# Kernel tuning notes

Measured on AMD Instinct MI355X. Metric: run time of the kernel, lower is better.

## Reference

```python
import jax, jax.numpy as jnp
import numpy as np


def setup_inputs() -> dict:
    key = jax.random.key(0)
    k1, k2, k3 = jax.random.split(key, 3)
    B, IN, H, OUT = 2048, 4096, 4096, 1024
    x = jax.random.normal(k1, (B, IN), dtype=jnp.float32)
    fc1_weight = jax.random.randint(k2, (H, IN), 0, 2).astype(jnp.int32)
    fc2_weight = jax.random.randint(k3, (OUT, H), 0, 2).astype(jnp.int32)
    return {"x": x, "fc1_weight": fc1_weight, "fc2_weight": fc2_weight, "threshold": 2048}


def _binary_popcount_matmul(a, w):
    # a: (B, K) in {0,1}, w: (N, K) in {0,1}
    # matches = sum_k 1 - (a XOR w) = a@w.T + (1-a)@(1-w).T  (identical math,
    # avoids materializing the (B, N, K) XNOR tensor the naive code builds)
    return jnp.einsum('bk,nk->bn', a, w) + jnp.einsum('bk,nk->bn', 1 - a, 1 - w)


def reference(x, fc1_weight, fc2_weight, threshold):
    xb = (x.reshape(x.shape[0], -1) >= 0).astype(jnp.int32)   # binarize input
    pc1 = _binary_popcount_matmul(xb, fc1_weight)              # (B, H) popcounts
    act1 = (pc1 >= threshold).astype(jnp.int32)                # threshold activation
    pc2 = _binary_popcount_matmul(act1, fc2_weight)            # (B, OUT) popcounts
    return pc2
```

## Files before the change

kernel.cpp:

```cpp
#include <hip/hip_runtime.h>
#include <stdint.h>

typedef int v4i  __attribute__((ext_vector_type(4)));
typedef int v16i __attribute__((ext_vector_type(16)));

__device__ __forceinline__ void gload_lds16(const void* g, void* l) {
    __builtin_amdgcn_global_load_lds(
        (const __attribute__((address_space(1))) void*)g,
        (__attribute__((address_space(3))) void*)l, 16, 0, 0);
}

template<typename T, bool ISFLOAT>
__global__ __launch_bounds__(512)
void pack_frag(const T* __restrict__ in, int8_t* __restrict__ F, int K) {
    __shared__ int8_t lbuf[32 * 1040];
    const int t  = threadIdx.x;
    const int db = blockIdx.y;
    const int c0 = blockIdx.x << 10;

    #pragma unroll
    for (int p = 0; p < 16; ++p) {
        int idx = p * 512 + t;
        int row = idx >> 8, c4 = idx & 255;
        uint32_t b;
        if constexpr (ISFLOAT) {
            const float4 v = *(const float4*)(in + (size_t)(db * 32 + row) * K + c0 + c4 * 4);
            b =  (v.x >= 0.0f ? 0x01u : 0xFFu)
              | ((v.y >= 0.0f ? 0x01u : 0xFFu) << 8)
              | ((v.z >= 0.0f ? 0x01u : 0xFFu) << 16)
              | ((v.w >= 0.0f ? 0x01u : 0xFFu) << 24);
        } else {
            const int4 v = *(const int4*)(in + (size_t)(db * 32 + row) * K + c0 + c4 * 4);
            b =  (v.x ? 0x01u : 0xFFu)
              | ((v.y ? 0x01u : 0xFFu) << 8)
              | ((v.z ? 0x01u : 0xFFu) << 16)
              | ((v.w ? 0x01u : 0xFFu) << 24);
        }
        *(uint32_t*)(lbuf + row * 1040 + c4 * 4) = b;
    }
    __syncthreads();

    const int s  = t >> 4;
    const int l0 = (t & 15) * 4;
    const int KC = K >> 5;
    int8_t* dst = F + ((size_t)db * KC + blockIdx.x * 32 + s) * 1024;
    #pragma unroll
    for (int li = 0; li < 4; ++li) {
        int l = l0 + li;
        uint4 v = *(const uint4*)(lbuf + (l & 31) * 1040 + s * 32 + (l >> 5) * 16);
        *(uint4*)(dst + l * 16) = v;
    }
}

__global__ __launch_bounds__(512, 1)
void bnn_l1_opt(const int8_t* __restrict__ Af,
                const int8_t* __restrict__ Bf,
                const int* __restrict__ thr_ptr,
                int8_t* __restrict__ actf)
{
    constexpr int KC  = 128;
    constexpr int NKT = 64;
    constexpr uint32_t BUFSZ = 24576;

    __shared__ int8_t lds[4 * 24576];

    const int tid  = threadIdx.x;
    const int lane = tid & 63;
    const int wv   = tid >> 6;
    const int wr   = wv >> 2, wc = wv & 3;

    const int g   = blockIdx.x;
    const int idx = g >> 3;
    const int bn  = (g & 7) * 2 + (idx >> 4);
    const int bm  = idx & 15;

    const int8_t* gsrc[3];
    uint32_t loff[3];
    #pragma unroll
    for (int c = 0; c < 3; ++c) {
        int s = c * 512 + tid;
        if (s < 512) {
            int R = s >> 7, kk = (s >> 6) & 1, ln = s & 63;
            gsrc[c] = Af + ((size_t)(bm * 4 + R) * KC + kk) * 1024 + ln * 16;
            loff[c] = (uint32_t)s * 16;
        } else {
            int s2 = s - 512;
            int Cb = s2 >> 7, kk = (s2 >> 6) & 1, ln = s2 & 63;
            gsrc[c] = Bf + ((size_t)(bn * 8 + Cb) * KC + kk) * 1024 + ln * 16;
            loff[c] = 8192u + (uint32_t)s2 * 16;
        }
    }

    auto issue3 = [&](uint32_t bufo) {
        gload_lds16(gsrc[0], lds + bufo + loff[0]); gsrc[0] += 2048;
        gload_lds16(gsrc[1], lds + bufo + loff[1]); gsrc[1] += 2048;
        gload_lds16(gsrc[2], lds + bufo + loff[2]); gsrc[2] += 2048;
    };

    v16i acc[2][2];
    #pragma unroll
    for (int i = 0; i < 2; ++i)
        #pragma unroll
        for (int j = 0; j < 2; ++j) acc[i][j] = {};

    issue3(0);
    issue3(BUFSZ);
    issue3(2 * BUFSZ);

#define KT_BODY(KT, P)                                                         \
    {                                                                          \
        const int kt_ = (KT);                                                  \
        if (kt_ < NKT - 2)       asm volatile("s_waitcnt vmcnt(6)" ::: "memory"); \
        else if (kt_ == NKT - 2) asm volatile("s_waitcnt vmcnt(3)" ::: "memory"); \
        else                     asm volatile("s_waitcnt vmcnt(0)" ::: "memory"); \
        __builtin_amdgcn_sched_barrier(0);                                     \
        __builtin_amdgcn_s_barrier();                                          \
        __builtin_amdgcn_sched_barrier(0);                                     \
        const int8_t* Ab = lds + (P) * 24576 + wr * 4096 + lane * 16;          \
        const int8_t* Bb = lds + (P) * 24576 + 8192 + wc * 4096 + lane * 16;   \
        v4i a00 = *(const v4i*)(Ab + 0);                                       \
        v4i a01 = *(const v4i*)(Ab + 1024);                                    \
        v4i a10 = *(const v4i*)(Ab + 2048);                                    \
        v4i a11 = *(const v4i*)(Ab + 3072);                                    \
        v4i b00 = *(const v4i*)(Bb + 0);                                       \
        v4i b01 = *(const v4i*)(Bb + 1024);                                    \
        v4i b10 = *(const v4i*)(Bb + 2048);                                    \
        v4i b11 = *(const v4i*)(Bb + 3072);                                    \
        if (kt_ + 3 < NKT) issue3(((P) + 3) % 4 * 24576u);                     \
        __builtin_amdgcn_sched_barrier(0);                                     \
        asm volatile("s_waitcnt lgkmcnt(0)" ::: "memory");                     \
        __builtin_amdgcn_sched_barrier(0);                                     \
        __builtin_amdgcn_s_setprio(1);                                         \
        acc[0][0] = __builtin_amdgcn_mfma_i32_32x32x32_i8(a00, b00, acc[0][0], 0, 0, 0); \
        acc[0][1] = __builtin_amdgcn_mfma_i32_32x32x32_i8(a00, b10, acc[0][1], 0, 0, 0); \
        acc[1][0] = __builtin_amdgcn_mfma_i32_32x32x32_i8(a10, b00, acc[1][0], 0, 0, 0); \
        acc[1][1] = __builtin_amdgcn_mfma_i32_32x32x32_i8(a10, b10, acc[1][1], 0, 0, 0); \
        acc[0][0] = __builtin_amdgcn_mfma_i32_32x32x32_i8(a01, b01, acc[0][0], 0, 0, 0); \
        acc[0][1] = __builtin_amdgcn_mfma_i32_32x32x32_i8(a01, b11, acc[0][1], 0, 0, 0); \
        acc[1][0] = __builtin_amdgcn_mfma_i32_32x32x32_i8(a11, b01, acc[1][0], 0, 0, 0); \
        acc[1][1] = __builtin_amdgcn_mfma_i32_32x32x32_i8(a11, b11, acc[1][1], 0, 0, 0); \
        __builtin_amdgcn_s_setprio(0);                                         \
        __builtin_amdgcn_sched_barrier(0);                                     \
    }

    #pragma unroll 1
    for (int kt0 = 0; kt0 < NKT; kt0 += 4) {
        KT_BODY(kt0 + 0, 0)
        KT_BODY(kt0 + 1, 1)
        KT_BODY(kt0 + 2, 2)
        KT_BODY(kt0 + 3, 3)
    }
#undef KT_BODY

    __syncthreads();
    const int thr = *thr_ptr;
    int8_t* bits = lds;
    #pragma unroll
    for (int i = 0; i < 2; ++i)
        #pragma unroll
        for (int j = 0; j < 2; ++j) {
            int dimb = wr * 64 + i * 32 + 4 * (lane >> 5);
            int gcl  = wc * 64 + j * 32 + (lane & 31);
            #pragma unroll
            for (int reg = 0; reg < 16; ++reg) {
                int dl = dimb + (reg & 3) + 8 * (reg >> 2);
                int match = (4096 + acc[i][j][reg]) >> 1;
                bits[dl * 272 + gcl] = (match >= thr) ? (int8_t)1 : (int8_t)-1;
            }
        }
    __syncthreads();
    const int s    = tid >> 4;
    const int dblk = s >> 3, kcl = s & 7;
    const int l0   = (tid & 15) * 4;
    int8_t* dst = actf + ((size_t)(bm * 4 + dblk) * KC + bn * 8 + kcl) * 1024;
    #pragma unroll
    for (int li = 0; li < 4; ++li) {
        int l = l0 + li;
        uint4 v = *(const uint4*)(bits + (dblk * 32 + (l & 31)) * 272
                                       + kcl * 32 + (l >> 5) * 16);
        *(uint4*)(dst + l * 16) = v;
    }
}

template<int WN>
__global__ __launch_bounds__(256, 1)
void bnn_mfma2(const int8_t* __restrict__ Af,
               const int8_t* __restrict__ Bf,
               int* __restrict__ out, int Nout)
{
    constexpr int KC     = 128;
    constexpr int NKT    = 64;
    constexpr int NBB    = 2 * WN;
    constexpr int ASLOTS = 512;
    constexpr int BSLOTS = 128 * NBB;
    constexpr int SLOTS  = ASLOTS + BSLOTS;
    constexpr int NLD    = SLOTS / 256;
    constexpr uint32_t BUFSZ = (uint32_t)SLOTS * 16;

    __shared__ int8_t lds[3][SLOTS * 16];

    const int tid  = threadIdx.x;
    const int lane = tid & 63;
    const int wv   = tid >> 6;
    const int wr   = wv >> 1, wc = wv & 1;

    const int g   = blockIdx.x;
    const int idx = g >> 3;
    const int bn  = (g & 7) * 2 + (idx >> 4);
    const int bm  = idx & 15;

    const int8_t* gsrc[NLD];
    uint32_t ldoff[NLD];
    #pragma unroll
    for (int i = 0; i < NLD; ++i) {
        int sbase = wv * 64 + 256 * i;
        ldoff[i] = (uint32_t)sbase * 16;
        const int8_t* base;
        if (sbase < ASLOTS) {
            int R = sbase >> 7, C = (sbase >> 6) & 1;
            base = Af + ((size_t)(bm * 4 + R) * KC + C) * 1024;
        } else {
            int s = sbase - ASLOTS;
            int R = s >> 7, C = (s >> 6) & 1;
            base = Bf + ((size_t)(bn * NBB + R) * KC + C) * 1024;
        }
        gsrc[i] = base + lane * 16;
    }

    auto stage = [&](int buf) {
        #pragma unroll
        for (int i = 0; i < NLD; ++i) {
            gload_lds16(gsrc[i], (int8_t*)lds + (uint32_t)buf * BUFSZ + ldoff[i]);
            gsrc[i] += 2048;
        }
    };

    v16i acc[2][WN];
    #pragma unroll
    for (int i = 0; i < 2; ++i)
        #pragma unroll
        for (int j = 0; j < WN; ++j) acc[i][j] = {};

    stage(0);
    stage(1);

    int cur = 0, nxt = 2;
    #pragma unroll 1
    for (int kt = 0; kt < NKT; ++kt) {
        if (kt < NKT - 1) asm volatile("s_waitcnt vmcnt(3)" ::: "memory");
        else              asm volatile("s_waitcnt vmcnt(0)" ::: "memory");
        __builtin_amdgcn_sched_barrier(0);
        __builtin_amdgcn_s_barrier();
        __builtin_amdgcn_sched_barrier(0);

        if (kt < NKT - 2) {
            stage(nxt);
            nxt = (nxt == 2) ? 0 : nxt + 1;
        }

        const int8_t* Al = lds[cur];
        const int8_t* Bl = lds[cur] + ASLOTS * 16;
        #pragma unroll
        for (int kc = 0; kc < 2; ++kc) {
            v4i af[2], bf[WN];
            #pragma unroll
            for (int i = 0; i < 2; ++i)
                af[i] = *(const v4i*)(Al + (((wr * 2 + i) * 2 + kc) * 64 + lane) * 16);
            #pragma unroll
            for (int j = 0; j < WN; ++j)
                bf[j] = *(const v4i*)(Bl + (((wc * WN + j) * 2 + kc) * 64 + lane) * 16);
            #pragma unroll
            for (int i = 0; i < 2; ++i)
                #pragma unroll
                for (int j = 0; j < WN; ++j)
                    acc[i][j] = __builtin_amdgcn_mfma_i32_32x32x32_i8(af[i], bf[j], acc[i][j], 0, 0, 0);
        }
        cur = (cur == 2) ? 0 : cur + 1;
    }

    #pragma unroll
    for (int i = 0; i < 2; ++i)
        #pragma unroll
        for (int j = 0; j < WN; ++j) {
            int gc = bn * (64 * WN) + wc * (32 * WN) + j * 32 + (lane & 31);
            #pragma unroll
            for (int reg = 0; reg < 16; ++reg) {
                int gr = bm * 128 + wr * 64 + i * 32
                       + (reg & 3) + 8 * (reg >> 2) + 4 * (lane >> 5);
                out[(size_t)gr * Nout + gc] = (4096 + acc[i][j][reg]) >> 1;
            }
        }
}

extern "C" void kernel_launch(void* const* d_in, const int* in_sizes, int n_in,
                              void* d_out, int out_size, void* d_ws, size_t ws_size,
                              hipStream_t stream) {
    const float* x   = (const float*)d_in[0];
    const int*   w1  = (const int*)d_in[1];
    const int*   w2  = (const int*)d_in[2];
    const int*   thr = (const int*)d_in[3];
    int* out = (int*)d_out;

    const int B = 2048, IN = 4096, H = 4096, OUT = 1024;
    uint8_t* ws = (uint8_t*)d_ws;

    int8_t* Af  = (int8_t*)(ws);
    int8_t* W1f = (int8_t*)(ws + ((size_t)8  << 20));
    int8_t* W2f = (int8_t*)(ws + ((size_t)24 << 20));
    int8_t* Act = (int8_t*)(ws + ((size_t)28 << 20));

    pack_frag<float, true ><<<dim3(IN / 1024, B   / 32), 512, 0, stream>>>(x,  Af,  IN);
    pack_frag<int,   false><<<dim3(IN / 1024, H   / 32), 512, 0, stream>>>(w1, W1f, IN);
    pack_frag<int,   false><<<dim3(H  / 1024, OUT / 32), 512, 0, stream>>>(w2, W2f, H);

    bnn_l1_opt<<<256, 512, 0, stream>>>(Af, W1f, thr, Act);
    bnn_mfma2<1><<<256, 256, 0, stream>>>(Act, W2f, out, OUT);
}
```

Before: 88.15 us.

## Retile layer-1 GEMM to 2-wave 128x128 blocks and halve pack_frag chunk

Layer-1 popcount GEMM moves from 512-thread blocks with 8 waves computing 256x128 tiles to 128-thread blocks with 2 waves, each wave computing 64x128 so that every A fragment is reused across 4 B fragments. The grid doubles to 512 blocks with 2 blocks per CU, and the LDS pipeline drops from 4 buffers to 3. The pack kernels now process 512-column chunks, launching twice as many smaller blocks with a simpler transpose. This trades fewer waves per CU and more accumulator registers for higher per-wave MFMA density and fewer barrier stalls, at some risk to latency hiding.

```diff
diff --git a/kernel.cpp b/kernel.cpp
--- a/kernel.cpp
+++ b/kernel.cpp
@@ -13,15 +13,15 @@
 template<typename T, bool ISFLOAT>
 __global__ __launch_bounds__(512)
 void pack_frag(const T* __restrict__ in, int8_t* __restrict__ F, int K) {
-    __shared__ int8_t lbuf[32 * 1040];
+    __shared__ int8_t lbuf[32 * 528];
     const int t  = threadIdx.x;
     const int db = blockIdx.y;
-    const int c0 = blockIdx.x << 10;
-
-    #pragma unroll
-    for (int p = 0; p < 16; ++p) {
+    const int c0 = blockIdx.x << 9;
+
+    #pragma unroll
+    for (int p = 0; p < 8; ++p) {
         int idx = p * 512 + t;
-        int row = idx >> 8, c4 = idx & 255;
+        int row = idx >> 7, c4 = idx & 127;
         uint32_t b;
         if constexpr (ISFLOAT) {
             const float4 v = *(const float4*)(in + (size_t)(db * 32 + row) * K + c0 + c4 * 4);
@@ -36,49 +36,46 @@
               | ((v.z ? 0x01u : 0xFFu) << 16)
               | ((v.w ? 0x01u : 0xFFu) << 24);
         }
-        *(uint32_t*)(lbuf + row * 1040 + c4 * 4) = b;
+        *(uint32_t*)(lbuf + row * 528 + c4 * 4) = b;
     }
     __syncthreads();
 
-    const int s  = t >> 4;
-    const int l0 = (t & 15) * 4;
+    const int s  = t >> 5;
+    const int l0 = t & 31;
     const int KC = K >> 5;
-    int8_t* dst = F + ((size_t)db * KC + blockIdx.x * 32 + s) * 1024;
-    #pragma unroll
-    for (int li = 0; li < 4; ++li) {
-        int l = l0 + li;
-        uint4 v = *(const uint4*)(lbuf + (l & 31) * 1040 + s * 32 + (l >> 5) * 16);
-        *(uint4*)(dst + l * 16) = v;
-    }
-}
-
-__global__ __launch_bounds__(512, 1)
-void bnn_l1_opt(const int8_t* __restrict__ Af,
-                const int8_t* __restrict__ Bf,
-                const int* __restrict__ thr_ptr,
-                int8_t* __restrict__ actf)
+    int8_t* dst = F + ((size_t)db * KC + (c0 >> 5) + s) * 1024;
+    uint4 v0 = *(const uint4*)(lbuf + l0 * 528 + s * 32);
+    uint4 v1 = *(const uint4*)(lbuf + l0 * 528 + s * 32 + 16);
+    *(uint4*)(dst + l0 * 16) = v0;
+    *(uint4*)(dst + (l0 + 32) * 16) = v1;
+}
+
+__global__ __launch_bounds__(128, 2)
+void bnn_l1_2w(const int8_t* __restrict__ Af,
+               const int8_t* __restrict__ Bf,
+               const int* __restrict__ thr_ptr,
+               int8_t* __restrict__ actf)
 {
     constexpr int KC  = 128;
     constexpr int NKT = 64;
-    constexpr uint32_t BUFSZ = 24576;
-
-    __shared__ int8_t lds[4 * 24576];
+    constexpr uint32_t BUFSZ = 16384;
+
+    __shared__ int8_t lds[3 * 16384];
 
     const int tid  = threadIdx.x;
     const int lane = tid & 63;
-    const int wv   = tid >> 6;
-    const int wr   = wv >> 2, wc = wv & 3;
+    const int wr   = tid >> 6;
 
     const int g   = blockIdx.x;
     const int idx = g >> 3;
-    const int bn  = (g & 7) * 2 + (idx >> 4);
+    const int bn  = (g & 7) * 4 + (idx >> 4);
     const int bm  = idx & 15;
 
-    const int8_t* gsrc[3];
-    uint32_t loff[3];
-    #pragma unroll
-    for (int c = 0; c < 3; ++c) {
-        int s = c * 512 + tid;
+    const int8_t* gsrc[8];
+    uint32_t loff[8];
+    #pragma unroll
+    for (int c = 0; c < 8; ++c) {
+        int s = c * 128 + tid;
         if (s < 512) {
             int R = s >> 7, kk = (s >> 6) & 1, ln = s & 63;
             gsrc[c] = Af + ((size_t)(bm * 4 + R) * KC + kk) * 1024 + ln * 16;
@@ -86,70 +83,77 @@
         } else {
             int s2 = s - 512;
             int Cb = s2 >> 7, kk = (s2 >> 6) & 1, ln = s2 & 63;
-            gsrc[c] = Bf + ((size_t)(bn * 8 + Cb) * KC + kk) * 1024 + ln * 16;
+            gsrc[c] = Bf + ((size_t)(bn * 4 + Cb) * KC + kk) * 1024 + ln * 16;
             loff[c] = 8192u + (uint32_t)s2 * 16;
         }
     }
-
-    auto issue3 = [&](uint32_t bufo) {
-        gload_lds16(gsrc[0], lds + bufo + loff[0]); gsrc[0] += 2048;
-        gload_lds16(gsrc[1], lds + bufo + loff[1]); gsrc[1] += 2048;
-        gload_lds16(gsrc[2], lds + bufo + loff[2]); gsrc[2] += 2048;
+    auto issue8 = [&](uint32_t bufo) {
+        #pragma unroll
+        for (int c = 0; c < 8; ++c) {
+            gload_lds16(gsrc[c], lds + bufo + loff[c]);
+            gsrc[c] += 2048;
+        }
     };
 
-    v16i acc[2][2];
+    v16i acc[2][4];
     #pragma unroll
     for (int i = 0; i < 2; ++i)
         #pragma unroll
-        for (int j = 0; j < 2; ++j) acc[i][j] = {};
-
-    issue3(0);
-    issue3(BUFSZ);
-    issue3(2 * BUFSZ);
+        for (int j = 0; j < 4; ++j) acc[i][j] = {};
+
+    issue8(0);
+    issue8(BUFSZ);
 
 #define KT_BODY(KT, P)                                                         \
     {                                                                          \
         const int kt_ = (KT);                                                  \
-        if (kt_ < NKT - 2)       asm volatile("s_waitcnt vmcnt(6)" ::: "memory"); \
-        else if (kt_ == NKT - 2) asm volatile("s_waitcnt vmcnt(3)" ::: "memory"); \
-        else                     asm volatile("s_waitcnt vmcnt(0)" ::: "memory"); \
+        if (kt_ < NKT - 1) asm volatile("s_waitcnt vmcnt(8)" ::: "memory");    \
+        else               asm volatile("s_waitcnt vmcnt(0)" ::: "memory");    \
         __builtin_amdgcn_sched_barrier(0);                                     \
         __builtin_amdgcn_s_barrier();                                          \
         __builtin_amdgcn_sched_barrier(0);                                     \
-        const int8_t* Ab = lds + (P) * 24576 + wr * 4096 + lane * 16;          \
-        const int8_t* Bb = lds + (P) * 24576 + 8192 + wc * 4096 + lane * 16;   \
+        const int8_t* Ab = lds + (P) * 16384 + wr * 4096 + lane * 16;          \
+        const int8_t* Bb = lds + (P) * 16384 + 8192 + lane * 16;               \
         v4i a00 = *(const v4i*)(Ab + 0);                                       \
         v4i a01 = *(const v4i*)(Ab + 1024);                                    \
         v4i a10 = *(const v4i*)(Ab + 2048);                                    \
         v4i a11 = *(const v4i*)(Ab + 3072);                                    \
-        v4i b00 = *(const v4i*)(Bb + 0);                                       \
-        v4i b01 = *(const v4i*)(Bb + 1024);                                    \
-        v4i b10 = *(const v4i*)(Bb + 2048);                                    \
-        v4i b11 = *(const v4i*)(Bb + 3072);                                    \
-        if (kt_ + 3 < NKT) issue3(((P) + 3) % 4 * 24576u);                     \
+        v4i b00 = *(const v4i*)(Bb + 0);    v4i b0k = *(const v4i*)(Bb + 1024);\
+        v4i b10 = *(const v4i*)(Bb + 2048); v4i b1k = *(const v4i*)(Bb + 3072);\
+        v4i b20 = *(const v4i*)(Bb + 4096); v4i b2k = *(const v4i*)(Bb + 5120);\
+        v4i b30 = *(const v4i*)(Bb + 6144); v4i b3k = *(const v4i*)(Bb + 7168);\
+        if (kt_ + 2 < NKT) issue8((uint32_t)(((P) + 2) % 3) * 16384u);         \
         __builtin_amdgcn_sched_barrier(0);                                     \
         asm volatile("s_waitcnt lgkmcnt(0)" ::: "memory");                     \
         __builtin_amdgcn_sched_barrier(0);                                     \
         __builtin_amdgcn_s_setprio(1);                                         \
         acc[0][0] = __builtin_amdgcn_mfma_i32_32x32x32_i8(a00, b00, acc[0][0], 0, 0, 0); \
         acc[0][1] = __builtin_amdgcn_mfma_i32_32x32x32_i8(a00, b10, acc[0][1], 0, 0, 0); \
+        acc[0][2] = __builtin_amdgcn_mfma_i32_32x32x32_i8(a00, b20, acc[0][2], 0, 0, 0); \
+        acc[0][3] = __builtin_amdgcn_mfma_i32_32x32x32_i8(a00, b30, acc[0][3], 0, 0, 0); \
         acc[1][0] = __builtin_amdgcn_mfma_i32_32x32x32_i8(a10, b00, acc[1][0], 0, 0, 0); \
         acc[1][1] = __builtin_amdgcn_mfma_i32_32x32x32_i8(a10, b10, acc[1][1], 0, 0, 0); \
-        acc[0][0] = __builtin_amdgcn_mfma_i32_32x32x32_i8(a01, b01, acc[0][0], 0, 0, 0); \
-        acc[0][1] = __builtin_amdgcn_mfma_i32_32x32x32_i8(a01, b11, acc[0][1], 0, 0, 0); \
-        acc[1][0] = __builtin_amdgcn_mfma_i32_32x32x32_i8(a11, b01, acc[1][0], 0, 0, 0); \
-        acc[1][1] = __builtin_amdgcn_mfma_i32_32x32x32_i8(a11, b11, acc[1][1], 0, 0, 0); \
+        acc[1][2] = __builtin_amdgcn_mfma_i32_32x32x32_i8(a10, b20, acc[1][2], 0, 0, 0); \
+        acc[1][3] = __builtin_amdgcn_mfma_i32_32x32x32_i8(a10, b30, acc[1][3], 0, 0, 0); \
+        acc[0][0] = __builtin_amdgcn_mfma_i32_32x32x32_i8(a01, b0k, acc[0][0], 0, 0, 0); \
+        acc[0][1] = __builtin_amdgcn_mfma_i32_32x32x32_i8(a01, b1k, acc[0][1], 0, 0, 0); \
+        acc[0][2] = __builtin_amdgcn_mfma_i32_32x32x32_i8(a01, b2k, acc[0][2], 0, 0, 0); \
+        acc[0][3] = __builtin_amdgcn_mfma_i32_32x32x32_i8(a01, b3k, acc[0][3], 0, 0, 0); \
+        acc[1][0] = __builtin_amdgcn_mfma_i32_32x32x32_i8(a11, b0k, acc[1][0], 0, 0, 0); \
+        acc[1][1] = __builtin_amdgcn_mfma_i32_32x32x32_i8(a11, b1k, acc[1][1], 0, 0, 0); \
+        acc[1][2] = __builtin_amdgcn_mfma_i32_32x32x32_i8(a11, b2k, acc[1][2], 0, 0, 0); \
+        acc[1][3] = __builtin_amdgcn_mfma_i32_32x32x32_i8(a11, b3k, acc[1][3], 0, 0, 0); \
         __builtin_amdgcn_s_setprio(0);                                         \
         __builtin_amdgcn_sched_barrier(0);                                     \
     }
 
     #pragma unroll 1
-    for (int kt0 = 0; kt0 < NKT; kt0 += 4) {
+    for (int kt0 = 0; kt0 < 63; kt0 += 3) {
         KT_BODY(kt0 + 0, 0)
         KT_BODY(kt0 + 1, 1)
         KT_BODY(kt0 + 2, 2)
-        KT_BODY(kt0 + 3, 3)
-    }
+    }
+    KT_BODY(63, 0)
 #undef KT_BODY
 
     __syncthreads();
@@ -158,25 +162,25 @@
     #pragma unroll
     for (int i = 0; i < 2; ++i)
         #pragma unroll
-        for (int j = 0; j < 2; ++j) {
+        for (int j = 0; j < 4; ++j) {
             int dimb = wr * 64 + i * 32 + 4 * (lane >> 5);
-            int gcl  = wc * 64 + j * 32 + (lane & 31);
+            int gcl  = j * 32 + (lane & 31);
             #pragma unroll
             for (int reg = 0; reg < 16; ++reg) {
                 int dl = dimb + (reg & 3) + 8 * (reg >> 2);
                 int match = (4096 + acc[i][j][reg]) >> 1;
-                bits[dl * 272 + gcl] = (match >= thr) ? (int8_t)1 : (int8_t)-1;
+                bits[dl * 144 + gcl] = (match >= thr) ? (int8_t)1 : (int8_t)-1;
             }
         }
     __syncthreads();
-    const int s    = tid >> 4;
-    const int dblk = s >> 3, kcl = s & 7;
-    const int l0   = (tid & 15) * 4;
-    int8_t* dst = actf + ((size_t)(bm * 4 + dblk) * KC + bn * 8 + kcl) * 1024;
-    #pragma unroll
-    for (int li = 0; li < 4; ++li) {
+    const int s    = tid >> 3;
+    const int dblk = s >> 2, kcl = s & 3;
+    const int l0   = (tid & 7) * 8;
+    int8_t* dst = actf + ((size_t)(bm * 4 + dblk) * KC + bn * 4 + kcl) * 1024;
+    #pragma unroll
+    for (int li = 0; li < 8; ++li) {
         int l = l0 + li;
-        uint4 v = *(const uint4*)(bits + (dblk * 32 + (l & 31)) * 272
+        uint4 v = *(const uint4*)(bits + (dblk * 32 + (l & 31)) * 144
                                        + kcl * 32 + (l >> 5) * 16);
         *(uint4*)(dst + l * 16) = v;
     }
@@ -309,10 +313,10 @@
     int8_t* W2f = (int8_t*)(ws + ((size_t)24 << 20));
     int8_t* Act = (int8_t*)(ws + ((size_t)28 << 20));
 
-    pack_frag<float, true ><<<dim3(IN / 1024, B   / 32), 512, 0, stream>>>(x,  Af,  IN);
-    pack_frag<int,   false><<<dim3(IN / 1024, H   / 32), 512, 0, stream>>>(w1, W1f, IN);
-    pack_frag<int,   false><<<dim3(H  / 1024, OUT / 32), 512, 0, stream>>>(w2, W2f, H);
-
-    bnn_l1_opt<<<256, 512, 0, stream>>>(Af, W1f, thr, Act);
+    pack_frag<float, true ><<<dim3(IN / 512, B   / 32), 512, 0, stream>>>(x,  Af,  IN);
+    pack_frag<int,   false><<<dim3(IN / 512, H   / 32), 512, 0, stream>>>(w1, W1f, IN);
+    pack_frag<int,   false><<<dim3(H  / 512, OUT / 32), 512, 0, stream>>>(w2, W2f, H);
+
+    bnn_l1_2w<<<512, 128, 0, stream>>>(Af, W1f, thr, Act);
     bnn_mfma2<1><<<256, 256, 0, stream>>>(Act, W2f, out, OUT);
 }
```

After: 92.02 us. 1.04x slower.
